# Kernel tuning notes

Measured on AMD Instinct MI355X. Metric: run time of the kernel, lower is better.

## Reference

```python
import jax, jax.numpy as jnp
import numpy as np

B, T, E, H = 4, 1024, 512, 8
DH = E // H  # head dim = 64


def setup_inputs() -> dict:
    key = jax.random.key(0)
    ks = jax.random.split(key, 6)
    s = 1.0 / np.sqrt(E)
    return {
        "q": jax.random.normal(ks[0], (B, T, E), dtype=jnp.float32),
        "kv": jax.random.normal(ks[1], (B, T, E), dtype=jnp.float32),
        "Wq": jax.random.normal(ks[2], (E, E), dtype=jnp.float32) * s,
        "Wk": jax.random.normal(ks[3], (E, E), dtype=jnp.float32) * s,
        "Wv": jax.random.normal(ks[4], (E, E), dtype=jnp.float32) * s,
        "Wo": jax.random.normal(ks[5], (E, E), dtype=jnp.float32) * s,
        "head_num": H,
    }


def _split_heads_dh(x, h):
    # einops 'b t (d h)' with h=head_num: head index is FASTEST in channel dim
    b, t, e = x.shape
    d = e // h
    return x.reshape(b, t, d, h).transpose(0, 3, 1, 2)  # (b, h, t, d)


def reference(q, kv, Wq, Wk, Wv, Wo, head_num):
    e = q.shape[-1]
    dk = (e // head_num) ** 0.5  # NOTE: multiplied, per original code

    qp = q @ Wq   # weights stored as (in, out); Linear(bias=False)
    kp = kv @ Wk
    vp = kv @ Wv

    query = _split_heads_dh(qp, head_num)  # (b, h, t, d)
    key = _split_heads_dh(kp, head_num)
    value = _split_heads_dh(vp, head_num)

    qf = jnp.fft.fftn(query, axes=(-2, -1))  # complex, over (t, d)
    kf = jnp.fft.fftn(key, axes=(-2, -1))

    # complex einsum, key NOT conjugated (faithful to torch source)
    energy = jnp.einsum("bhid,bhjd->bhij", qf, kf) * dk
    energy = jnp.fft.ifftn(energy, axes=(-2, -1)).real  # (b, h, t, t)

    attention = jax.nn.softmax(energy, axis=-1)
    out = jnp.einsum("bhij,bhjd->bhid", attention, value)  # (b, h, t, d)

    # einops 'b h t d -> b t (h d)': head index SLOWEST in output channel dim
    b, h, t, d = out.shape
    out = out.transpose(0, 2, 1, 3).reshape(b, t, h * d)
    return out @ Wo
```

## Files before the change

kernel.cpp:

```cpp
#include <hip/hip_runtime.h>
#include <math.h>

#define BB 4
#define TT 1024
#define EE 512
#define HH 8
#define DD 64
#define BT (BB * TT)

typedef _Float16 f16;
typedef __attribute__((ext_vector_type(8))) _Float16 f16x8;
typedef __attribute__((ext_vector_type(4))) float f32x4;

__device__ __forceinline__ void dma16(const f16* g, char* l) {
    __builtin_amdgcn_global_load_lds(
        (const __attribute__((address_space(1))) void*)g,
        (__attribute__((address_space(3))) void*)l, 16, 0, 0);
}

__global__ __launch_bounds__(256) void prep_k(
    const float* __restrict__ q, const float* __restrict__ kv,
    const float* __restrict__ Wq, const float* __restrict__ Wk,
    const float* __restrict__ Wv, const float* __restrict__ Wo,
    f16* __restrict__ wqh, f16* __restrict__ wql,
    f16* __restrict__ wkh, f16* __restrict__ wkl,
    f16* __restrict__ wvh, f16* __restrict__ woh,
    f16* __restrict__ qAhi, f16* __restrict__ qAlo,
    f16* __restrict__ kvAhi, f16* __restrict__ kvAlo) {
    const int t = threadIdx.x;
    const int y = blockIdx.y;
    if (y < 4) {
        int idx = blockIdx.x * 256 + t;
        int k = idx & (EE - 1);
        int n = idx >> 9;
        if (y == 0) {
            float v = Wq[k * EE + n] * 512.0f;
            f16 hi = (f16)v;
            wqh[n * EE + k] = hi;
            wql[n * EE + k] = (f16)(v - (float)hi);
        } else if (y == 1) {
            int d = n >> 3, h = n & 7;
            int sn = (((DD - d) & (DD - 1)) << 3) | h;
            float v = Wk[k * EE + sn];
            f16 hi = (f16)v;
            wkh[n * EE + k] = hi;
            wkl[n * EE + k] = (f16)(v - (float)hi);
        } else if (y == 2) {
            wvh[n * EE + k] = (f16)Wv[k * EE + n];
        } else {
            woh[n * EE + k] = (f16)Wo[k * EE + n];
        }
    } else {
        const float* src = (y == 4) ? q : kv;
        f16* dh = (y == 4) ? qAhi : kvAhi;
        f16* dl = (y == 4) ? qAlo : kvAlo;
        int base = (blockIdx.x * 256 + t) * 8;
        float4 a = *(const float4*)&src[base];
        float4 c = *(const float4*)&src[base + 4];
        float xs[8] = {a.x, a.y, a.z, a.w, c.x, c.y, c.z, c.w};
        f16x8 hi, lo;
#pragma unroll
        for (int e = 0; e < 8; ++e) {
            f16 hh = (f16)xs[e];
            hi[e] = hh;
            lo[e] = (f16)(xs[e] - (float)hh);
        }
        *(f16x8*)&dh[base] = hi;
        *(f16x8*)&dl[base] = lo;
    }
}

__global__ __launch_bounds__(256) void proj_k(
    const f16* __restrict__ qAhi, const f16* __restrict__ qAlo,
    const f16* __restrict__ kvAhi, const f16* __restrict__ kvAlo,
    const f16* __restrict__ wqh, const f16* __restrict__ wql,
    const f16* __restrict__ wkh, const f16* __restrict__ wkl,
    const f16* __restrict__ wvh,
    f16* __restrict__ qhi, f16* __restrict__ qlo,
    f16* __restrict__ kthi, f16* __restrict__ ktlo, f16* __restrict__ vP) {
    __shared__ __align__(16) f16 A_s[2][2][128][32];
    __shared__ __align__(16) f16 W_s[2][3][64][32];
    f16 (*Ep)[136] = reinterpret_cast<f16(*)[136]>(&A_s[0][0][0][0]);

    const int t = threadIdx.x;
    const int w = t >> 6, l = t & 63;
    const int wm = w >> 1, wn = w & 1;
    const int fr = l & 15, fc = l >> 4;
    const int m0b = blockIdx.x * 128;
    const int n0b = blockIdx.y * 64;
    const int z   = blockIdx.z;

    const f16* AH = z ? kvAhi : qAhi;
    const f16* AL = z ? kvAlo : qAlo;
    const f16* WH = z ? wkh : wqh;
    const f16* WL = z ? wkl : wql;

    f32x4 accK[4][2], accV[4][2];
#pragma unroll
    for (int i = 0; i < 4; ++i)
#pragma unroll
        for (int j = 0; j < 2; ++j) {
            accK[i][j] = f32x4{0.f, 0.f, 0.f, 0.f};
            accV[i][j] = f32x4{0.f, 0.f, 0.f, 0.f};
        }

    auto stageDMA = [&](int bf, int k0) {
#pragma unroll
        for (int i = 0; i < 2; ++i) {
            int slot = (i * 4 + w) * 64 + l;
            int r = slot >> 2, qv = slot & 3;
            const f16* gh = AH + (size_t)(m0b + r) * EE + k0 + qv * 8;
            const f16* gl = AL + (size_t)(m0b + r) * EE + k0 + qv * 8;
            dma16(gh, (char*)&A_s[bf][0][0][0] + (i * 4 + w) * 1024);
            dma16(gl, (char*)&A_s[bf][1][0][0] + (i * 4 + w) * 1024);
        }
        {
            int slot = w * 64 + l;
            int r = slot >> 2, qv = slot & 3;
            const f16* g0 = WH + (size_t)(n0b + r) * EE + k0 + qv * 8;
            const f16* g1 = WL + (size_t)(n0b + r) * EE + k0 + qv * 8;
            dma16(g0, (char*)&W_s[bf][0][0][0] + w * 1024);
            dma16(g1, (char*)&W_s[bf][1][0][0] + w * 1024);
            if (z) {
                const f16* g2 = wvh + (size_t)(n0b + r) * EE + k0 + qv * 8;
                dma16(g2, (char*)&W_s[bf][2][0][0] + w * 1024);
            }
        }
    };

    auto comp = [&](int bf) {
        f16x8 Ahf[4], Alf[4], Bh[2], Bl[2], Bv[2];
#pragma unroll
        for (int mi = 0; mi < 4; ++mi) {
            Ahf[mi] = *(const f16x8*)&A_s[bf][0][wm * 64 + mi * 16 + fr][fc * 8];
            Alf[mi] = *(const f16x8*)&A_s[bf][1][wm * 64 + mi * 16 + fr][fc * 8];
        }
#pragma unroll
        for (int nj = 0; nj < 2; ++nj) {
            Bh[nj] = *(const f16x8*)&W_s[bf][0][wn * 32 + nj * 16 + fr][fc * 8];
            Bl[nj] = *(const f16x8*)&W_s[bf][1][wn * 32 + nj * 16 + fr][fc * 8];
            if (z) Bv[nj] = *(const f16x8*)&W_s[bf][2][wn * 32 + nj * 16 + fr][fc * 8];
        }
        __builtin_amdgcn_s_setprio(1);
#pragma unroll
        for (int mi = 0; mi < 4; ++mi)
#pragma unroll
            for (int nj = 0; nj < 2; ++nj) {
                accK[mi][nj] = __builtin_amdgcn_mfma_f32_16x16x32_f16(
                    Ahf[mi], Bh[nj], accK[mi][nj], 0, 0, 0);
                accK[mi][nj] = __builtin_amdgcn_mfma_f32_16x16x32_f16(
                    Ahf[mi], Bl[nj], accK[mi][nj], 0, 0, 0);
                accK[mi][nj] = __builtin_amdgcn_mfma_f32_16x16x32_f16(
                    Alf[mi], Bh[nj], accK[mi][nj], 0, 0, 0);
                if (z)
                    accV[mi][nj] = __builtin_amdgcn_mfma_f32_16x16x32_f16(
                        Ahf[mi], Bv[nj], accV[mi][nj], 0, 0, 0);
            }
        __builtin_amdgcn_s_setprio(0);
    };

    stageDMA(0, 0);
    __syncthreads();
    int cur = 0;
    for (int ks = 0; ks < 16; ++ks) {
        if (ks < 15) stageDMA(cur ^ 1, (ks + 1) * 32);
        comp(cur);
        __syncthreads();
        cur ^= 1;
    }

    const int d0  = n0b >> 3;
    const int kfc = d0 >> 5;
    const int lg2 = (d0 >> 3) & 3;
#pragma unroll
    for (int mi = 0; mi < 4; ++mi)
#pragma unroll
        for (int nj = 0; nj < 2; ++nj)
#pragma unroll
            for (int r = 0; r < 4; ++r)
                Ep[wn * 32 + nj * 16 + fr][wm * 64 + mi * 16 + fc * 4 + r] =
                    (f16)accK[mi][nj][r];
    __syncthreads();
#pragma unroll
    for (int i = 0; i < 4; ++i) {
        int task = t * 4 + i;
        int mr = task >> 3, h = task & 7;
        f16x8 v;
#pragma unroll
        for (int d = 0; d < 8; ++d) v[d] = Ep[8 * d + h][mr];
        if (z == 0) {
            *(f16x8*)&qhi[((size_t)h * BT + m0b + mr) * DD + d0] = v;
        } else {
            int mg = m0b + mr;
            int bb = mg >> 10, key = mg & 1023;
            size_t off = ((((((size_t)h * BB + bb) * 16 + (key >> 6)) * 4 +
                            ((key >> 4) & 3)) * 2 + kfc) * 64 +
                          lg2 * 16 + (key & 15)) * 8;
            *(f16x8*)&kthi[off] = v;
        }
    }
    __syncthreads();
#pragma unroll
    for (int mi = 0; mi < 4; ++mi)
#pragma unroll
        for (int nj = 0; nj < 2; ++nj)
#pragma unroll
            for (int r = 0; r < 4; ++r) {
                float x = accK[mi][nj][r];
                f16 hh = (f16)x;
                Ep[wn * 32 + nj * 16 + fr][wm * 64 + mi * 16 + fc * 4 + r] =
                    (f16)(x - (float)hh);
            }
    __syncthreads();
#pragma unroll
    for (int i = 0; i < 4; ++i) {
        int task = t * 4 + i;
        int mr = task >> 3, h = task & 7;
        f16x8 v;
#pragma unroll
        for (int d = 0; d < 8; ++d) v[d] = Ep[8 * d + h][mr];
        if (z == 0) {
            *(f16x8*)&qlo[((size_t)h * BT + m0b + mr) * DD + d0] = v;
        } else {
            int mg = m0b + mr;
            int bb = mg >> 10, key = mg & 1023;
            size_t off = ((((((size_t)h * BB + bb) * 16 + (key >> 6)) * 4 +
                            ((key >> 4) & 3)) * 2 + kfc) * 64 +
                          lg2 * 16 + (key & 15)) * 8;
            *(f16x8*)&ktlo[off] = v;
        }
    }
    if (z) {
        __syncthreads();
#pragma unroll
        for (int mi = 0; mi < 4; ++mi)
#pragma unroll
            for (int nj = 0; nj < 2; ++nj)
#pragma unroll
                for (int r = 0; r < 4; ++r)
                    Ep[wn * 32 + nj * 16 + fr][wm * 64 + mi * 16 + fc * 4 + r] =
                        (f16)accV[mi][nj][r];
        __syncthreads();
#pragma unroll
        for (int i = 0; i < 4; ++i) {
            int task = t * 4 + i;
            int mg = task & 15, nn = task >> 4;
            int h = nn & 7, dl = nn >> 3;
            int d = d0 + dl;
            int koff = m0b + mg * 8;
            int tile = koff >> 6;
            int kf   = (koff >> 5) & 1;
            int lgv  = (koff >> 3) & 3;
            int dvt  = d >> 4, lqd = d & 15;
            f16x8 v = *(const f16x8*)&Ep[nn][mg * 8];
            size_t off = (((((size_t)h * 64 + tile) * 2 + kf) * 4 + dvt) * 64 +
                          lgv * 16 + lqd) * 8;
            *(f16x8*)&vP[off] = v;
        }
    }
}

__global__ __launch_bounds__(256) void outmm_k(const f16* __restrict__ Af,
                                               const f16* __restrict__ WThi,
                                               float* __restrict__ out) {
    __shared__ __align__(16) f16 Ah_s[2][64][72];
    __shared__ __align__(16) f16 Wh_s[2][64][72];

    const int t = threadIdx.x;
    const int w = t >> 6, l = t & 63;
    const int wm = w >> 1, wn = w & 1;
    const int fr = l & 15, fc = l >> 4;
    const int m0b = blockIdx.x * 64;
    const int n0b = blockIdx.y * 64;
    const int sr = t >> 2, sch = t & 3;

    f32x4 acc[2][2];
#pragma unroll
    for (int i = 0; i < 2; ++i)
#pragma unroll
        for (int j = 0; j < 2; ++j) acc[i][j] = f32x4{0.f, 0.f, 0.f, 0.f};

    f16x8 af[2], wf[2];
    auto loadAB = [&](int k0) {
#pragma unroll
        for (int i = 0; i < 2; ++i) {
            af[i] = *(const f16x8*)&Af[(size_t)(m0b + sr) * EE + k0 + sch * 16 + i * 8];
            wf[i] = *(const f16x8*)&WThi[(size_t)(n0b + sr) * EE + k0 + sch * 16 + i * 8];
        }
    };
    auto stage = [&](int bf) {
#pragma unroll
        for (int i = 0; i < 2; ++i) {
            *(f16x8*)&Ah_s[bf][sr][sch * 16 + i * 8] = af[i];
            *(f16x8*)&Wh_s[bf][sr][sch * 16 + i * 8] = wf[i];
        }
    };

    loadAB(0);
    stage(0);
    __syncthreads();
    int cur = 0;
    for (int ks = 0; ks < 8; ++ks) {
        if (ks < 7) loadAB((ks + 1) * 64);
        f16x8 Ahf[2][2], Bhf[2][2];
#pragma unroll
        for (int mi = 0; mi < 2; ++mi)
#pragma unroll
            for (int kb = 0; kb < 2; ++kb)
                Ahf[mi][kb] =
                    *(const f16x8*)&Ah_s[cur][wm * 32 + mi * 16 + fr][kb * 32 + fc * 8];
#pragma unroll
        for (int nj = 0; nj < 2; ++nj)
#pragma unroll
            for (int kb = 0; kb < 2; ++kb)
                Bhf[nj][kb] =
                    *(const f16x8*)&Wh_s[cur][wn * 32 + nj * 16 + fr][kb * 32 + fc * 8];
        __builtin_amdgcn_s_setprio(1);
#pragma unroll
        for (int mi = 0; mi < 2; ++mi)
#pragma unroll
            for (int nj = 0; nj < 2; ++nj)
#pragma unroll
                for (int kb = 0; kb < 2; ++kb)
                    acc[mi][nj] = __builtin_amdgcn_mfma_f32_16x16x32_f16(
                        Ahf[mi][kb], Bhf[nj][kb], acc[mi][nj], 0, 0, 0);
        __builtin_amdgcn_s_setprio(0);
        if (ks < 7) stage(cur ^ 1);
        __syncthreads();
        cur ^= 1;
    }

#pragma unroll
    for (int mi = 0; mi < 2; ++mi)
#pragma unroll
        for (int nj = 0; nj < 2; ++nj)
#pragma unroll
            for (int r = 0; r < 4; ++r)
                out[(size_t)(m0b + wm * 32 + mi * 16 + fc * 4 + r) * EE +
                    n0b + wn * 32 + nj * 16 + fr] = acc[mi][nj][r];
}

__global__ __launch_bounds__(256) void attn_mfma_k(const f16* __restrict__ qhiP,
    const f16* __restrict__ qloP, const f16* __restrict__ kthiP,
    const f16* __restrict__ ktloP, const f16* __restrict__ vP,
    f16* __restrict__ ctx) {
    __shared__ __align__(16) f16 Pl[4][16][88];

    const int bid = blockIdx.x;
    const int swz = (bid & 7) * 64 + (bid >> 3);
    const int bx = swz & 15;
    const int h  = (swz >> 4) & 7;
    const int b  = swz >> 7;

    const int t  = threadIdx.x;
    const int w  = t >> 6;
    const int l  = t & 63;
    const int lg = l >> 4;
    const int lq = l & 15;
    const int q0 = bx * 64 + w * 16;
    const size_t plane = ((size_t)h * BT + (size_t)b * TT) * DD;

    f16x8 Qhi[2], Qlo[2];
#pragma unroll
    for (int kf = 0; kf < 2; ++kf) {
        size_t qo = plane + (size_t)(q0 + lq) * DD + kf * 32 + lg * 8;
        Qhi[kf] = *(const f16x8*)&qhiP[qo];
        Qlo[kf] = *(const f16x8*)&qloP[qo];
    }

    f32x4 Oacc[4];
#pragma unroll
    for (int i = 0; i < 4; ++i) Oacc[i] = f32x4{0.f, 0.f, 0.f, 0.f};
    float m = -1e30f, lsum = 0.f;

    const f16* khb = kthiP + (((size_t)h * BB + b) << 16);
    const f16* klb = ktloP + (((size_t)h * BB + b) << 16);

    f16x8 kA[4], kB[4];
    auto LK = [&](int kt64, int kt, f16x8 (&s)[4]) {
        size_t o = ((size_t)kt64 * 4 + kt) * 1024 + l * 8;
        s[0] = *(const f16x8*)&khb[o];
        s[1] = *(const f16x8*)&khb[o + 512];
        s[2] = *(const f16x8*)&klb[o];
        s[3] = *(const f16x8*)&klb[o + 512];
    };
    auto QK1 = [&](const f16x8 (&s)[4]) -> f32x4 {
        f32x4 c = f32x4{0.f, 0.f, 0.f, 0.f};
        __builtin_amdgcn_s_setprio(1);
        c = __builtin_amdgcn_mfma_f32_16x16x32_f16(s[0], Qhi[0], c, 0, 0, 0);
        c = __builtin_amdgcn_mfma_f32_16x16x32_f16(s[0], Qlo[0], c, 0, 0, 0);
        c = __builtin_amdgcn_mfma_f32_16x16x32_f16(s[2], Qhi[0], c, 0, 0, 0);
        c = __builtin_amdgcn_mfma_f32_16x16x32_f16(s[1], Qhi[1], c, 0, 0, 0);
        c = __builtin_amdgcn_mfma_f32_16x16x32_f16(s[1], Qlo[1], c, 0, 0, 0);
        c = __builtin_amdgcn_mfma_f32_16x16x32_f16(s[3], Qhi[1], c, 0, 0, 0);
        __builtin_amdgcn_s_setprio(0);
        return c;
    };

    f16x8 bvA[2][4], bvB[2][4];
    auto loadBV = [&](int tile, f16x8 (&bv)[2][4]) {
        const f16* tb = vP + ((size_t)h * 64 + b * 16 + tile) * 4096;
#pragma unroll
        for (int kf = 0; kf < 2; ++kf)
#pragma unroll
            for (int dvt = 0; dvt < 4; ++dvt)
                bv[kf][dvt] = *(const f16x8*)&tb[((kf * 4 + dvt) * 64 + l) * 8];
    };

    auto SMPV = [&](const f32x4 (&Sc)[4], const f16x8 (&bv)[2][4]) {
        float sv[16];
#pragma unroll
        for (int kt = 0; kt < 4; ++kt)
#pragma unroll
            for (int r = 0; r < 4; ++r) sv[kt * 4 + r] = Sc[kt][r];
        float tm = sv[0];
#pragma unroll
        for (int i = 1; i < 16; ++i) tm = fmaxf(tm, sv[i]);
        tm = fmaxf(tm, __shfl_xor(tm, 16));
        tm = fmaxf(tm, __shfl_xor(tm, 32));

        bool skip = __all(tm <= m + 8.0f);
        float Mn = m, corr = 1.0f;
        if (!skip) {
            Mn = fmaxf(m, tm);
            corr = __expf(m - Mn);
        }
        float ps = 0.f;
        f16 ph[16];
#pragma unroll
        for (int i = 0; i < 16; ++i) {
            float p = __expf(sv[i] - Mn);
            ps += p;
            ph[i] = (f16)p;
        }
        ps += __shfl_xor(ps, 16);
        ps += __shfl_xor(ps, 32);
        if (skip) {
            lsum += ps;
        } else {
            lsum = lsum * corr + ps;
            m = Mn;
        }

#pragma unroll
        for (int kt = 0; kt < 4; ++kt)
#pragma unroll
            for (int rp = 0; rp < 4; rp += 2) {
                union { f16 h; unsigned short u; } u0, u1;
                u0.h = ph[kt * 4 + rp]; u1.h = ph[kt * 4 + rp + 1];
                unsigned int pk = ((unsigned int)u1.u << 16) | u0.u;
                *(unsigned int*)&Pl[w][lq][kt * 16 + lg * 4 + rp] = pk;
            }

        if (!skip) {
            float cq[4];
#pragma unroll
            for (int r = 0; r < 4; ++r) cq[r] = __shfl(corr, lg * 4 + r);
#pragma unroll
            for (int dvt = 0; dvt < 4; ++dvt)
#pragma unroll
                for (int r = 0; r < 4; ++r) Oacc[dvt][r] *= cq[r];
        }

        __builtin_amdgcn_s_setprio(1);
#pragma unroll
        for (int kf = 0; kf < 2; ++kf) {
            f16x8 pa = *(const f16x8*)&Pl[w][lq][kf * 32 + lg * 8];
#pragma unroll
            for (int dvt = 0; dvt < 4; ++dvt)
                Oacc[dvt] = __builtin_amdgcn_mfma_f32_16x16x32_f16(
                    pa, bv[kf][dvt], Oacc[dvt], 0, 0, 0);
        }
        __builtin_amdgcn_s_setprio(0);
    };

    LK(0, 0, kA);
    loadBV(0, bvA);
    f32x4 Sc[4];

    for (int tile = 0; tile < 16; tile += 2) {
        LK(tile, 1, kB);      Sc[0] = QK1(kA);
        LK(tile, 2, kA);      Sc[1] = QK1(kB);
        LK(tile, 3, kB);      Sc[2] = QK1(kA);
        LK(tile + 1, 0, kA);  Sc[3] = QK1(kB);
        loadBV(tile + 1, bvB);
        SMPV(Sc, bvA);
        LK(tile + 1, 1, kB);  Sc[0] = QK1(kA);
        LK(tile + 1, 2, kA);  Sc[1] = QK1(kB);
        LK(tile + 1, 3, kB);  Sc[2] = QK1(kA);
        if (tile + 2 < 16) LK(tile + 2, 0, kA);
        Sc[3] = QK1(kB);
        if (tile + 2 < 16) loadBV(tile + 2, bvA);
        SMPV(Sc, bvB);
    }

    float linv = 1.0f / lsum;
    float lq4[4];
#pragma unroll
    for (int r = 0; r < 4; ++r) lq4[r] = __shfl(linv, lg * 4 + r);
#pragma unroll
    for (int r = 0; r < 4; ++r) {
        f16* crow = ctx + (size_t)(b * TT + q0 + lg * 4 + r) * EE + h * DD;
#pragma unroll
        for (int dvt = 0; dvt < 4; ++dvt)
            crow[dvt * 16 + lq] = (f16)(Oacc[dvt][r] * lq4[r]);
    }
}

extern "C" void kernel_launch(void* const* d_in, const int* in_sizes, int n_in,
                              void* d_out, int out_size, void* d_ws, size_t ws_size,
                              hipStream_t stream) {
    const float* q  = (const float*)d_in[0];
    const float* kv = (const float*)d_in[1];
    const float* Wq = (const float*)d_in[2];
    const float* Wk = (const float*)d_in[3];
    const float* Wv = (const float*)d_in[4];
    const float* Wo = (const float*)d_in[5];
    float* out = (float*)d_out;

    f16* ws = (f16*)d_ws;
    const size_t PL  = (size_t)HH * BT * DD;
    const size_t WPL = (size_t)EE * EE;
    f16* qhi   = ws + 0 * PL;
    f16* qlo   = ws + 1 * PL;
    f16* kthi  = ws + 2 * PL;
    f16* ktlo  = ws + 3 * PL;
    f16* vPck  = ws + 4 * PL;
    f16* ctx   = ws + 5 * PL;
    f16* qAhi  = ws + 6 * PL;
    f16* qAlo  = ws + 7 * PL;
    f16* kvAhi = ws + 8 * PL;
    f16* kvAlo = ws + 9 * PL;
    f16* wqh = ws + 10 * PL;
    f16* wql = wqh + 1 * WPL;
    f16* wkh = wqh + 2 * WPL;
    f16* wkl = wqh + 3 * WPL;
    f16* wvh = wqh + 4 * WPL;
    f16* woh = wqh + 5 * WPL;

    prep_k<<<dim3(1024, 6), dim3(256), 0, stream>>>(
        q, kv, Wq, Wk, Wv, Wo, wqh, wql, wkh, wkl, wvh, woh,
        qAhi, qAlo, kvAhi, kvAlo);

    proj_k<<<dim3(BT / 128, EE / 64, 2), dim3(256), 0, stream>>>(
        qAhi, qAlo, kvAhi, kvAlo, wqh, wql, wkh, wkl, wvh,
        qhi, qlo, kthi, ktlo, vPck);

    attn_mfma_k<<<dim3(512), dim3(256), 0, stream>>>(
        qhi, qlo, kthi, ktlo, vPck, ctx);

    outmm_k<<<dim3(BT / 64, EE / 64), dim3(256), 0, stream>>>(ctx, woh, out);
}
```

Measured before the change: 77.31 us.

## Stage K/V tiles in LDS via async DMA shared across 8 waves

The attention kernel now uses 512-thread blocks, each covering 128 query rows (8 waves). K-hi, K-lo and V tiles go into double-buffered LDS through global_load_lds DMA instead of being loaded from global memory into registers separately by every wave. This raises reuse of each K/V tile across more query rows and cuts global traffic and register pressure. In exchange the block count halves to 256, which may underfill the GPU, and each tile step adds a block-wide barrier and extra LDS reads.

```diff
diff --git a/kernel.cpp b/kernel.cpp
--- a/kernel.cpp
+++ b/kernel.cpp
@@ -340,24 +340,26 @@
                     n0b + wn * 32 + nj * 16 + fr] = acc[mi][nj][r];
 }
 
-__global__ __launch_bounds__(256) void attn_mfma_k(const f16* __restrict__ qhiP,
+__global__ __launch_bounds__(512) void attn_mfma_k(const f16* __restrict__ qhiP,
     const f16* __restrict__ qloP, const f16* __restrict__ kthiP,
     const f16* __restrict__ ktloP, const f16* __restrict__ vP,
     f16* __restrict__ ctx) {
-    __shared__ __align__(16) f16 Pl[4][16][88];
+    __shared__ __align__(16) f16 KhiL[2][4096];
+    __shared__ __align__(16) f16 KloL[2][4096];
+    __shared__ __align__(16) f16 VL[2][4096];
+    __shared__ __align__(16) f16 Pl[8][16][88];
 
     const int bid = blockIdx.x;
-    const int swz = (bid & 7) * 64 + (bid >> 3);
-    const int bx = swz & 15;
-    const int h  = (swz >> 4) & 7;
-    const int b  = swz >> 7;
+    const int bx = (bid >> 3) & 7;
+    const int h  = bid & 7;
+    const int b  = bid >> 6;
 
     const int t  = threadIdx.x;
     const int w  = t >> 6;
     const int l  = t & 63;
     const int lg = l >> 4;
     const int lq = l & 15;
-    const int q0 = bx * 64 + w * 16;
+    const int q0 = bx * 128 + w * 16;
     const size_t plane = ((size_t)h * BT + (size_t)b * TT) * DD;
 
     f16x8 Qhi[2], Qlo[2];
@@ -375,39 +377,37 @@
 
     const f16* khb = kthiP + (((size_t)h * BB + b) << 16);
     const f16* klb = ktloP + (((size_t)h * BB + b) << 16);
-
-    f16x8 kA[4], kB[4];
-    auto LK = [&](int kt64, int kt, f16x8 (&s)[4]) {
-        size_t o = ((size_t)kt64 * 4 + kt) * 1024 + l * 8;
-        s[0] = *(const f16x8*)&khb[o];
-        s[1] = *(const f16x8*)&khb[o + 512];
-        s[2] = *(const f16x8*)&klb[o];
-        s[3] = *(const f16x8*)&klb[o + 512];
-    };
-    auto QK1 = [&](const f16x8 (&s)[4]) -> f32x4 {
+    const f16* vtb = vP + ((size_t)h * 64 + b * 16) * 4096;
+
+    auto stageDMA = [&](int bf, int tile) {
+        const f16* ks = khb + (size_t)tile * 4096 + t * 8;
+        const f16* ls = klb + (size_t)tile * 4096 + t * 8;
+        const f16* vs = vtb + (size_t)tile * 4096 + t * 8;
+        dma16(ks, (char*)&KhiL[bf][0] + w * 1024);
+        dma16(ls, (char*)&KloL[bf][0] + w * 1024);
+        dma16(vs, (char*)&VL[bf][0] + w * 1024);
+    };
+
+    auto QK1 = [&](int bf, int kt) -> f32x4 {
+        const f16* bh = &KhiL[bf][kt * 1024];
+        const f16* bl = &KloL[bf][kt * 1024];
+        f16x8 s0 = *(const f16x8*)&bh[l * 8];
+        f16x8 s1 = *(const f16x8*)&bh[512 + l * 8];
+        f16x8 s2 = *(const f16x8*)&bl[l * 8];
+        f16x8 s3 = *(const f16x8*)&bl[512 + l * 8];
         f32x4 c = f32x4{0.f, 0.f, 0.f, 0.f};
         __builtin_amdgcn_s_setprio(1);
-        c = __builtin_amdgcn_mfma_f32_16x16x32_f16(s[0], Qhi[0], c, 0, 0, 0);
-        c = __builtin_amdgcn_mfma_f32_16x16x32_f16(s[0], Qlo[0], c, 0, 0, 0);
-        c = __builtin_amdgcn_mfma_f32_16x16x32_f16(s[2], Qhi[0], c, 0, 0, 0);
-        c = __builtin_amdgcn_mfma_f32_16x16x32_f16(s[1], Qhi[1], c, 0, 0, 0);
-        c = __builtin_amdgcn_mfma_f32_16x16x32_f16(s[1], Qlo[1], c, 0, 0, 0);
-        c = __builtin_amdgcn_mfma_f32_16x16x32_f16(s[3], Qhi[1], c, 0, 0, 0);
+        c = __builtin_amdgcn_mfma_f32_16x16x32_f16(s0, Qhi[0], c, 0, 0, 0);
+        c = __builtin_amdgcn_mfma_f32_16x16x32_f16(s0, Qlo[0], c, 0, 0, 0);
+        c = __builtin_amdgcn_mfma_f32_16x16x32_f16(s2, Qhi[0], c, 0, 0, 0);
+        c = __builtin_amdgcn_mfma_f32_16x16x32_f16(s1, Qhi[1], c, 0, 0, 0);
+        c = __builtin_amdgcn_mfma_f32_16x16x32_f16(s1, Qlo[1], c, 0, 0, 0);
+        c = __builtin_amdgcn_mfma_f32_16x16x32_f16(s3, Qhi[1], c, 0, 0, 0);
         __builtin_amdgcn_s_setprio(0);
         return c;
     };
 
-    f16x8 bvA[2][4], bvB[2][4];
-    auto loadBV = [&](int tile, f16x8 (&bv)[2][4]) {
-        const f16* tb = vP + ((size_t)h * 64 + b * 16 + tile) * 4096;
-#pragma unroll
-        for (int kf = 0; kf < 2; ++kf)
-#pragma unroll
-            for (int dvt = 0; dvt < 4; ++dvt)
-                bv[kf][dvt] = *(const f16x8*)&tb[((kf * 4 + dvt) * 64 + l) * 8];
-    };
-
-    auto SMPV = [&](const f32x4 (&Sc)[4], const f16x8 (&bv)[2][4]) {
+    auto SMPV = [&](int bf, const f32x4 (&Sc)[4]) {
         float sv[16];
 #pragma unroll
         for (int kt = 0; kt < 4; ++kt)
@@ -467,31 +467,26 @@
         for (int kf = 0; kf < 2; ++kf) {
             f16x8 pa = *(const f16x8*)&Pl[w][lq][kf * 32 + lg * 8];
 #pragma unroll
-            for (int dvt = 0; dvt < 4; ++dvt)
+            for (int dvt = 0; dvt < 4; ++dvt) {
+                f16x8 bv = *(const f16x8*)&VL[bf][((kf * 4 + dvt) * 64 + l) * 8];
                 Oacc[dvt] = __builtin_amdgcn_mfma_f32_16x16x32_f16(
-                    pa, bv[kf][dvt], Oacc[dvt], 0, 0, 0);
+                    pa, bv, Oacc[dvt], 0, 0, 0);
+            }
         }
         __builtin_amdgcn_s_setprio(0);
     };
 
-    LK(0, 0, kA);
-    loadBV(0, bvA);
-    f32x4 Sc[4];
-
-    for (int tile = 0; tile < 16; tile += 2) {
-        LK(tile, 1, kB);      Sc[0] = QK1(kA);
-        LK(tile, 2, kA);      Sc[1] = QK1(kB);
-        LK(tile, 3, kB);      Sc[2] = QK1(kA);
-        LK(tile + 1, 0, kA);  Sc[3] = QK1(kB);
-        loadBV(tile + 1, bvB);
-        SMPV(Sc, bvA);
-        LK(tile + 1, 1, kB);  Sc[0] = QK1(kA);
-        LK(tile + 1, 2, kA);  Sc[1] = QK1(kB);
-        LK(tile + 1, 3, kB);  Sc[2] = QK1(kA);
-        if (tile + 2 < 16) LK(tile + 2, 0, kA);
-        Sc[3] = QK1(kB);
-        if (tile + 2 < 16) loadBV(tile + 2, bvA);
-        SMPV(Sc, bvB);
+    stageDMA(0, 0);
+    __syncthreads();
+    int cur = 0;
+    for (int tile = 0; tile < 16; ++tile) {
+        if (tile + 1 < 16) stageDMA(cur ^ 1, tile + 1);
+        f32x4 Sc[4];
+#pragma unroll
+        for (int kt = 0; kt < 4; ++kt) Sc[kt] = QK1(cur, kt);
+        SMPV(cur, Sc);
+        __syncthreads();
+        cur ^= 1;
     }
 
     float linv = 1.0f / lsum;
@@ -546,7 +541,7 @@
         qAhi, qAlo, kvAhi, kvAlo, wqh, wql, wkh, wkl, wvh,
         qhi, qlo, kthi, ktlo, vPck);
 
-    attn_mfma_k<<<dim3(512), dim3(256), 0, stream>>>(
+    attn_mfma_k<<<dim3(256), dim3(512), 0, stream>>>(
         qhi, qlo, kthi, ktlo, vPck, ctx);
 
     outmm_k<<<dim3(BT / 64, EE / 64), dim3(256), 0, stream>>>(ctx, woh, out);
```

Result: faster. 75.64 us, median of 2 (-2.2%).
